# Optimization experiments

Hardware: AMD Instinct MI355X
Metric: run time of the kernel (lower is better)

## Reference

```python
import jax, jax.numpy as jnp
import numpy as np

P = 7  # pool_size (module fast path: pool_size=7, C=512)


def setup_inputs() -> dict:
    key = jax.random.key(0)
    B, N, H, W, C = 2, 64, 38, 38, 512
    k1, k2, k3, k4, k5 = jax.random.split(key, 5)
    feature_map = jax.random.normal(k1, (B, H, W, C), dtype=jnp.float32)
    # ROI = (y, x, h, w) in integer feature-map coordinates, h,w >= P so every
    # pooling cell is non-empty and the bin boundaries partition the ROI exactly
    # (the original's max(size,1) clamp is then a no-op).
    h = jax.random.randint(k2, (B, N), P, H + 1, dtype=jnp.int32)
    w = jax.random.randint(k3, (B, N), P, W + 1, dtype=jnp.int32)
    y = jnp.floor(jax.random.uniform(k4, (B, N)) * (H - h + 1).astype(jnp.float32)).astype(jnp.int32)
    x = jnp.floor(jax.random.uniform(k5, (B, N)) * (W - w + 1).astype(jnp.float32)).astype(jnp.int32)
    rois = jnp.stack([y, x, h, w], axis=-1)
    return {"feature_map": feature_map, "rois": rois}


def _roi_pool(feature_map, rois, pool_size=P):
    # feature_map: [B,H,W,C] float, rois: [B,N,4] int (y, x, h, w)
    B, H, W, C = feature_map.shape
    N = rois.shape[1]
    PP = pool_size * pool_size
    y0 = rois[..., 0][:, :, None]  # [B,N,1]
    x0 = rois[..., 1][:, :, None]
    h = rois[..., 2][:, :, None]
    w = rois[..., 3][:, :, None]

    # For a pixel at relative row r inside an ROI of height h (h >= pool_size),
    # its bin b is the largest b with floor(b*h/pool_size) <= r, i.e.
    # b = (pool_size*r + pool_size-1) // h  -- identical to the original's
    # [floor(b*h/P), floor((b+1)*h/P)) partition (last bin end = h).
    rel_y = jnp.arange(H, dtype=jnp.int32)[None, None, :] - y0  # [B,N,H]
    rel_x = jnp.arange(W, dtype=jnp.int32)[None, None, :] - x0  # [B,N,W]
    ybin = (pool_size * rel_y + (pool_size - 1)) // jnp.maximum(h, 1)
    xbin = (pool_size * rel_x + (pool_size - 1)) // jnp.maximum(w, 1)
    valid_y = (rel_y >= 0) & (rel_y < h)  # [B,N,H]
    valid_x = (rel_x >= 0) & (rel_x < w)  # [B,N,W]

    cell = ybin[:, :, :, None] * pool_size + xbin[:, :, None, :]  # [B,N,H,W]
    valid = valid_y[:, :, :, None] & valid_x[:, :, None, :]
    cell = jnp.where(valid, cell, PP)  # PP = dump cell for out-of-ROI pixels

    roi_id = jnp.arange(B * N, dtype=jnp.int32).reshape(B, N, 1, 1)
    seg = (roi_id * (PP + 1) + cell).reshape(-1)  # [B*N*H*W]

    # Values: feature map broadcast over the ROI axis -> one fused segment-max.
    vals = jnp.broadcast_to(feature_map[:, None], (B, N, H, W, C)).reshape(-1, C)
    pooled = jax.ops.segment_max(vals, seg, num_segments=B * N * (PP + 1))
    pooled = pooled.reshape(B, N, PP + 1, C)[:, :, :PP]  # drop dump cell
    return pooled.reshape(B, N, pool_size, pool_size, C)


def reference(feature_map, rois):
    return _roi_pool(feature_map, rois)
```

## Files before the change

### kernel.cpp

```cpp
#include <hip/hip_runtime.h>
#include <hip/hip_bf16.h>
#include <math.h>

#define RB 2
#define RN 64
#define RH 38
#define RW 38
#define RC 512
#define RP 7
#define CELLS (RB * RN * RP * RP)
#define CPI (RN * RP * RP)
#define PPI (CPI / 2)

__device__ __forceinline__ float4 max4(float4 a, float4 b) {
  return make_float4(fmaxf(a.x, b.x), fmaxf(a.y, b.y), fmaxf(a.z, b.z),
                     fmaxf(a.w, b.w));
}

__global__ __launch_bounds__(256) void roi_pool_kernel(
    const float* __restrict__ fm, const int* __restrict__ rois,
    float* __restrict__ out) {
  int wv = threadIdx.x >> 6;
  int lane = threadIdx.x & 63;
  int half = wv & 1;

  int bx = blockIdx.x;
  int x = bx & 7;
  int j = bx >> 3;
  int img = x >> 2;
  int pair = img * PPI + ((j << 2) | (x & 3));
  int cell = pair * 2 + (wv >> 1);

  int px = cell % RP;
  int t = cell / RP;
  int py = t % RP;
  t /= RP;
  int b = t / RN;

  int rid = __builtin_amdgcn_readfirstlane(t);
  const int4 rv = *(const int4*)(rois + (rid << 2));
  int y0 = rv.x, x0 = rv.y, h = rv.z, w = rv.w;

  int ys = (py * h) / RP, ye = ((py + 1) * h) / RP;
  int xs = (px * w) / RP, xe = ((px + 1) * w) / RP;
  int bw = xe - xs;
  int cnt = bw * (ye - ys);

  const float4* p =
      (const float4*)(fm +
                      (size_t)((b * RH + y0 + ys) * RW + x0 + xs) * RC) +
      (half << 6) + lane;
  const int pixstep = RC / 4;
  const int wrapstep = (RW - bw) * (RC / 4);

#define STEP() \
  { p += pixstep; if (--xrem == 0) { xrem = bw; p += wrapstep; } }

  float4 m = make_float4(-INFINITY, -INFINITY, -INFINITY, -INFINITY);
  int xrem = bw;

  float4 a0, a1, a2, a3;
  a0 = *p;
  if (cnt > 1) { STEP(); a1 = *p; }
  if (cnt > 2) { STEP(); a2 = *p; }
  if (cnt > 3) { STEP(); a3 = *p; }
  int rem = cnt - 4;
  while (rem > 0) {
    m = max4(m, a0);
    STEP(); a0 = *p; --rem;
    if (rem > 0) {
      m = max4(m, a1);
      STEP(); a1 = *p; --rem;
    }
    if (rem > 0) {
      m = max4(m, a2);
      STEP(); a2 = *p; --rem;
    }
    if (rem > 0) {
      m = max4(m, a3);
      STEP(); a3 = *p; --rem;
    }
  }
  m = max4(m, a0);
  if (cnt > 1) m = max4(m, a1);
  if (cnt > 2) m = max4(m, a2);
  if (cnt > 3) m = max4(m, a3);
#undef STEP

  float4* o = (float4*)(out + (size_t)cell * RC) + (half << 6) + lane;
  *o = m;
}

extern "C" void kernel_launch(void* const* d_in, const int* in_sizes, int n_in,
                              void* d_out, int out_size, void* d_ws, size_t ws_size,
                              hipStream_t stream) {
  const float* fm = (const float*)d_in[0];
  const int* rois = (const int*)d_in[1];
  float* out = (float*)d_out;

  roi_pool_kernel<<<CELLS / 2, 256, 0, stream>>>(fm, rois, out);
}
```

Before: 68.40 us.

## Stage per-image channel slices in LDS and pool all ROI cells from shared memory

Each block now loads an 8-channel slice of the whole 38x38 feature map for one image into LDS, padded to spread accesses across banks. Its threads then compute pooled maxima for every cell of 16 ROIs from LDS, instead of each block reading its cell's pixels straight from global memory. This is meant to remove the heavy redundant global traffic from overlapping ROIs re-reading the same pixels. In exchange, global loads are narrow 32-byte strided segments, the grid shrinks to 512 blocks, and the per-thread loops over variable-sized bins can diverge and hit LDS bank conflicts.

```diff
diff --git a/kernel.cpp b/kernel.cpp
--- a/kernel.cpp
+++ b/kernel.cpp
@@ -1,5 +1,4 @@
 #include <hip/hip_runtime.h>
-#include <hip/hip_bf16.h>
 #include <math.h>
 
 #define RB 2
@@ -8,87 +7,99 @@
 #define RW 38
 #define RC 512
 #define RP 7
-#define CELLS (RB * RN * RP * RP)
-#define CPI (RN * RP * RP)
-#define PPI (CPI / 2)
+#define NPIX (RH * RW)
+#define NCH 8
+#define GRAN (NPIX * 2)
+#define LDS_SLOTS (GRAN + (GRAN >> 3) + 8)
+#define NTASK (16 * 49 * 2)
 
 __device__ __forceinline__ float4 max4(float4 a, float4 b) {
-  return make_float4(fmaxf(a.x, b.x), fmaxf(a.y, b.y), fmaxf(a.z, b.z),
-                     fmaxf(a.w, b.w));
+  return make_float4(fmaxf(a.x, b.x), fmaxf(a.y, b.y),
+                     fmaxf(a.z, b.z), fmaxf(a.w, b.w));
 }
 
 __global__ __launch_bounds__(256) void roi_pool_kernel(
     const float* __restrict__ fm, const int* __restrict__ rois,
     float* __restrict__ out) {
-  int wv = threadIdx.x >> 6;
-  int lane = threadIdx.x & 63;
-  int half = wv & 1;
+  __shared__ float4 lds[LDS_SLOTS];
 
   int bx = blockIdx.x;
-  int x = bx & 7;
+  int xid = bx & 7;
   int j = bx >> 3;
-  int img = x >> 2;
-  int pair = img * PPI + ((j << 2) | (x & 3));
-  int cell = pair * 2 + (wv >> 1);
+  int img = xid >> 2;
+  int u = (xid & 3) | (j << 2);
+  int chunk = u & 63;
+  int rq = u >> 6;
 
-  int px = cell % RP;
-  int t = cell / RP;
-  int py = t % RP;
-  t /= RP;
-  int b = t / RN;
+  const float* base = fm + (size_t)img * NPIX * RC + chunk * NCH;
 
-  int rid = __builtin_amdgcn_readfirstlane(t);
-  const int4 rv = *(const int4*)(rois + (rid << 2));
-  int y0 = rv.x, x0 = rv.y, h = rv.z, w = rv.w;
-
-  int ys = (py * h) / RP, ye = ((py + 1) * h) / RP;
-  int xs = (px * w) / RP, xe = ((px + 1) * w) / RP;
-  int bw = xe - xs;
-  int cnt = bw * (ye - ys);
-
-  const float4* p =
-      (const float4*)(fm +
-                      (size_t)((b * RH + y0 + ys) * RW + x0 + xs) * RC) +
-      (half << 6) + lane;
-  const int pixstep = RC / 4;
-  const int wrapstep = (RW - bw) * (RC / 4);
-
-#define STEP() \
-  { p += pixstep; if (--xrem == 0) { xrem = bw; p += wrapstep; } }
-
-  float4 m = make_float4(-INFINITY, -INFINITY, -INFINITY, -INFINITY);
-  int xrem = bw;
-
-  float4 a0, a1, a2, a3;
-  a0 = *p;
-  if (cnt > 1) { STEP(); a1 = *p; }
-  if (cnt > 2) { STEP(); a2 = *p; }
-  if (cnt > 3) { STEP(); a3 = *p; }
-  int rem = cnt - 4;
-  while (rem > 0) {
-    m = max4(m, a0);
-    STEP(); a0 = *p; --rem;
-    if (rem > 0) {
-      m = max4(m, a1);
-      STEP(); a1 = *p; --rem;
+  {
+    int s = threadIdx.x;
+#pragma unroll
+    for (int it = 0; it < 11; ++it) {
+      int p = s >> 1, q = s & 1;
+      float4 v = *(const float4*)(base + p * RC + (q << 2));
+      lds[s + (s >> 3)] = v;
+      s += 256;
     }
-    if (rem > 0) {
-      m = max4(m, a2);
-      STEP(); a2 = *p; --rem;
-    }
-    if (rem > 0) {
-      m = max4(m, a3);
-      STEP(); a3 = *p; --rem;
+    if (s < GRAN) {
+      int p = s >> 1, q = s & 1;
+      float4 v = *(const float4*)(base + p * RC + (q << 2));
+      lds[s + (s >> 3)] = v;
     }
   }
-  m = max4(m, a0);
-  if (cnt > 1) m = max4(m, a1);
-  if (cnt > 2) m = max4(m, a2);
-  if (cnt > 3) m = max4(m, a3);
-#undef STEP
+  __syncthreads();
 
-  float4* o = (float4*)(out + (size_t)cell * RC) + (half << 6) + lane;
-  *o = m;
+  for (int it = 0; it < 7; ++it) {
+    int t = threadIdx.x + (it << 8);
+    bool valid = t < NTASK;
+    int tc = valid ? t : (NTASK - 1);
+    int ci = tc >> 1, q = tc & 1;
+    int rl = ci / 49;
+    int cir = ci - rl * 49;
+    int py = cir / 7, px = cir - py * 7;
+    int roi_g = (img << 6) | (rq << 4) | rl;
+    const int4 rv = *(const int4*)(rois + (roi_g << 2));
+    int y0 = rv.x, x0 = rv.y, h = rv.z, w = rv.w;
+
+    int ys = (py * h) / RP, ye = ((py + 1) * h) / RP;
+    int xs = (px * w) / RP, xe = ((px + 1) * w) / RP;
+    int bw = xe - xs;
+    int cnt = bw * (ye - ys);
+
+    int g = (((y0 + ys) * RW + (x0 + xs)) << 1) | q;
+    int gwrap = (RW - bw) << 1;
+
+#define LD(dst) { dst = lds[g + (g >> 3)]; }
+#define ADV() { g += 2; if (--xrem == 0) { xrem = bw; g += gwrap; } }
+
+    float4 m = make_float4(-INFINITY, -INFINITY, -INFINITY, -INFINITY);
+    int xrem = bw;
+    float4 a0, a1, a2, a3;
+    LD(a0);
+    if (cnt > 1) { ADV(); LD(a1); }
+    if (cnt > 2) { ADV(); LD(a2); }
+    if (cnt > 3) { ADV(); LD(a3); }
+    int rem = cnt - 4;
+    while (rem > 0) {
+      m = max4(m, a0); ADV(); LD(a0); --rem;
+      if (rem > 0) { m = max4(m, a1); ADV(); LD(a1); --rem; }
+      if (rem > 0) { m = max4(m, a2); ADV(); LD(a2); --rem; }
+      if (rem > 0) { m = max4(m, a3); ADV(); LD(a3); --rem; }
+    }
+    m = max4(m, a0);
+    if (cnt > 1) m = max4(m, a1);
+    if (cnt > 2) m = max4(m, a2);
+    if (cnt > 3) m = max4(m, a3);
+#undef LD
+#undef ADV
+
+    if (valid) {
+      float4* o = (float4*)(out + (size_t)(roi_g * 49 + cir) * RC +
+                            chunk * NCH) + q;
+      *o = m;
+    }
+  }
 }
 
 extern "C" void kernel_launch(void* const* d_in, const int* in_sizes, int n_in,
@@ -98,5 +109,5 @@
   const int* rois = (const int*)d_in[1];
   float* out = (float*)d_out;
 
-  roi_pool_kernel<<<CELLS / 2, 256, 0, stream>>>(fm, rois, out);
+  roi_pool_kernel<<<512, 256, 0, stream>>>(fm, rois, out);
 }
```

Result: slower. 78.34 us (+14.5%).
